# Kernel optimization log

Measured on AMD Instinct MI355X. Metric: run time of the kernel, lower is better.

Reference implementation:

```python
import jax, jax.numpy as jnp
import numpy as np

C = 3.0e8
WAVE_LAMBDA = 0.0038
PI = float(np.pi)


def _grid(size, resolution, x_val):
    edge_left = [-i for i in range(1, size, 2)][::-1]
    edge_right = [i for i in range(1, size, 2)]
    edge = edge_left + edge_right
    if size % 2 == 1:
        edge = [i for i in range(-(size - 1), size, 2)]
    edge = np.array(edge, dtype=np.float32) * resolution / 2.0
    wx, wy = np.meshgrid(edge, edge)
    wz = np.zeros((size, size), dtype=np.float32)
    pos = np.stack((wz, wx, wy), 2).reshape(size * size, 3).astype(np.float32)
    pos[:, 0] = x_val
    return pos


def setup_inputs() -> dict:
    key = jax.random.key(0)
    k1, k2, k3 = jax.random.split(key, 3)
    lam = WAVE_LAMBDA
    f = np.arange(77e9, 81e9 + 1e9, 1e9, dtype=np.float32)  # [5]
    tx = np.array([[0, -8 * lam, 0], [0, -6 * lam, 0], [0, -4 * lam, 0], [0, -2 * lam, 0],
                   [0, 0, 0], [0, 2 * lam, 0], [0, 4 * lam, 0], [0, 6 * lam, 0], [0, 8 * lam, 0],
                   [0, -2.5 * lam, -3 * lam], [0, -3.0 * lam, -2 * lam], [0, -3.5 * lam, -0.5 * lam]],
                  dtype=np.float32)  # [12,3]
    rx = np.array([[0, -16 * lam, -0.066], [0, -15.5 * lam, -0.066], [0, -15 * lam, -0.066],
                   [0, -14.5 * lam, -0.066], [0, -10.5 * lam, -0.066], [0, -10 * lam, -0.066],
                   [0, -9.5 * lam, -0.066], [0, -9 * lam, -0.066], [0, 7 * lam, -0.066],
                   [0, 7.5 * lam, -0.066], [0, 8 * lam, -0.066], [0, 8.5 * lam, -0.066],
                   [0, 9 * lam, -0.066], [0, 9.5 * lam, -0.066], [0, 10 * lam, -0.066],
                   [0, 10.5 * lam, -0.066]], dtype=np.float32)  # [16,3]
    meta = _grid(60, 0.0015, 0.1)     # [3600,3]
    scene = _grid(20, 0.0015, 0.3)    # [400,3] (resolution reassigned to 0.0015 in torch init)
    # trainable params
    meta_theta = jax.random.uniform(k1, (3600, 1), jnp.float32,
                                    minval=-PI, maxval=20 * PI / 180.0)
    w = jax.random.normal(k2, (5, 6, 12), jnp.float32)
    T = jax.random.normal(k3, (400, 128), jnp.float32)
    return {"T": T, "w": w, "meta_theta": meta_theta, "f": jnp.asarray(f),
            "tx_positions": jnp.asarray(tx), "rx_positions": jnp.asarray(rx),
            "meta_positions": jnp.asarray(meta), "scene_positions": jnp.asarray(scene)}


def _channel(locs_start, locs_end, f):
    # pairwise distance [Ns,Ne], then complex channel [F,Ns,Ne]
    d = jnp.linalg.norm(locs_start[:, None, :] - locs_end[None, :, :], axis=2)
    return (0.001 / d ** 2) * jnp.exp(-1j * 2 * PI * f[:, None, None] * d / C)


def reference(T, w, meta_theta, f, tx_positions, rx_positions, meta_positions, scene_positions):
    theta = jnp.clip(meta_theta, -PI, 20 * PI / 180.0)[:, 0]   # [M]
    phase = jnp.exp(1j * theta)                                # [M]
    pri = jnp.exp(1j * w)                                      # [F,6,Tx]
    H1 = _channel(tx_positions, meta_positions, f)             # [F,Tx,M]
    H2 = _channel(meta_positions, scene_positions, f)          # [F,M,S]
    H3 = _channel(scene_positions, meta_positions, f)          # [F,S,M]
    H4 = _channel(meta_positions, rx_positions, f)             # [F,M,Rx]
    A = jnp.einsum('fkt,ftm->fkm', pri, H1)                    # [F,6,M]
    A = A * phase[None, None, :]
    A = jnp.einsum('fkm,fms->fks', A, H2)                      # [F,6,S]
    # diag_embed(A) @ H3  ==  per-row scaling of H3 (no dense SxS diag needed)
    A = A[..., None] * H3[:, None, :, :]                       # [F,6,S,M]
    A = A * phase[None, None, None, :]
    A = jnp.einsum('fksm,fmr->fksr', A, H4)                    # [F,6,S,Rx]
    A = jnp.transpose(A, (3, 0, 1, 2))                         # [Rx,F,6,S]
    A = jnp.tile(A, (1, 1, 12, 1))                             # [Rx,F,72,S]
    A = A.reshape(-1, A.shape[3])                              # [Rx*F*72, S]
    T_complex = T.astype(jnp.complex64)
    mic_data = A @ T_complex                                   # [Rx*F*72, B]
    s_A = jnp.concatenate([A.real, A.imag], axis=0)            # [2*Rx*F*72, S]
    s_mic = jnp.concatenate([mic_data.real, mic_data.imag], axis=0)[..., None]
    return (s_A, s_mic)
```

## Files before the change

kernel.cpp:

```cpp
#include <hip/hip_runtime.h>
#include <hip/hip_bf16.h>
#include <math.h>

#define F_N 5
#define K_N 6
#define T_N 12
#define M_N 3600
#define S_N 400
#define R_N 16
#define B_N 128

#define PI_F 3.14159265358979f
#define CLIP_HI 0.3490658503988659f
#define NEG_TWO_PI_OVER_C (-6.283185307179586f / 3.0e8f)
#define INV_TWO_PI 0.15915494309189535f

#define SA_BASE   0
#define MIC_BASE  4608000

#define NK 113
#define KP (NK * 32)
#define SPK 8
#define W_ELEMS  (5 * 48 * KP)
#define C_ELEMS  (SPK * 5 * 48 * 800)
#define WS_NEED  ((size_t)W_ELEMS * 2 + (size_t)C_ELEMS * 4)

typedef __attribute__((ext_vector_type(8))) short bf16x8;
typedef __attribute__((ext_vector_type(4))) short s16x4;
typedef __attribute__((ext_vector_type(4))) float f32x4;

__device__ __forceinline__ void fast_sincos(float x, float* s, float* c) {
    float r = x * INV_TWO_PI;
    r -= floorf(r);
    *s = __builtin_amdgcn_sinf(r);
    *c = __builtin_amdgcn_cosf(r);
}

__device__ __forceinline__ ushort f2bf(float x) {
    unsigned u = __float_as_uint(x);
    unsigned r = u + 0x7fffu + ((u >> 16) & 1u);
    return (ushort)(r >> 16);
}


__global__ __launch_bounds__(256) void stage_kernel(
    const float* __restrict__ w, const float* __restrict__ meta_theta,
    const float* __restrict__ fin, const float* __restrict__ txp,
    const float* __restrict__ rxp, const float* __restrict__ metap,
    __hip_bfloat16* __restrict__ Wbf)
{
    const int tid = threadIdx.x;
    const int blk = blockIdx.x;

    __shared__ float pri[K_N * T_N * 2];
    __shared__ float txs[T_N * 3];
    __shared__ float rxs[R_N * 3];
    const int f = blk / 15;
    const int mblk = blk % 15;

    if (tid < K_N * T_N) {
        float sv, cv; fast_sincos(w[f * (K_N * T_N) + tid], &sv, &cv);
        pri[tid * 2] = cv; pri[tid * 2 + 1] = sv;
    }
    if (tid >= 64 && tid < 64 + T_N * 3) txs[tid - 64] = txp[tid - 64];
    if (tid >= 128 && tid < 128 + R_N * 3) rxs[tid - 128] = rxp[tid - 128];
    __syncthreads();

    const int m = mblk * 256 + tid;
    if (m >= KP) return;
    __hip_bfloat16* wb = Wbf + ((size_t)(f * NK + (m >> 5)) * 48) * 32 + (m & 31);

    if (m >= M_N) {
        for (int row = 0; row < 48; ++row) wb[row * 32] = __float2bfloat16(0.f);
        return;
    }

    const float px = metap[m * 3 + 0];
    const float py = metap[m * 3 + 1];
    const float pz = metap[m * 3 + 2];
    const float coef = NEG_TWO_PI_OVER_C * fin[f];

    float th = meta_theta[m];
    th = fminf(fmaxf(th, -PI_F), CLIP_HI);
    float phs, phc; fast_sincos(th, &phs, &phc);

    float hre[T_N], him[T_N];
#pragma unroll
    for (int t = 0; t < T_N; ++t) {
        float dx = txs[t * 3 + 0] - px, dy = txs[t * 3 + 1] - py, dz = txs[t * 3 + 2] - pz;
        float d = sqrtf(dx * dx + dy * dy + dz * dz);
        float amp = 1e-3f / (d * d);
        float sv, cv; fast_sincos(coef * d, &sv, &cv);
        hre[t] = amp * cv; him[t] = amp * sv;
    }
#pragma unroll
    for (int k = 0; k < K_N; ++k) {
        float ar = 0.f, ai = 0.f;
#pragma unroll
        for (int t = 0; t < T_N; ++t) {
            float pr = pri[(k * T_N + t) * 2], pim = pri[(k * T_N + t) * 2 + 1];
            ar += pr * hre[t] - pim * him[t];
            ai += pr * him[t] + pim * hre[t];
        }
        wb[k * 32]        = __float2bfloat16(ar * phc - ai * phs);
        wb[(22 + k) * 32] = __float2bfloat16(ar * phs + ai * phc);
    }
#pragma unroll
    for (int r = 0; r < R_N; ++r) {
        float dx = rxs[r * 3 + 0] - px, dy = rxs[r * 3 + 1] - py, dz = rxs[r * 3 + 2] - pz;
        float d = sqrtf(dx * dx + dy * dy + dz * dz);
        float amp = 1e-3f / (d * d);
        float sv, cv; fast_sincos(coef * d, &sv, &cv);
        float cr = amp * cv, ci = amp * sv;
        wb[(6 + r) * 32]  = __float2bfloat16(cr * phc - ci * phs);
        wb[(28 + r) * 32] = __float2bfloat16(cr * phs + ci * phc);
    }
#pragma unroll
    for (int row = 44; row < 48; ++row) wb[row * 32] = __float2bfloat16(0.f);
}

__global__ __launch_bounds__(128) void gemm_fused_kernel(
    const ushort* __restrict__ Wbf, const float* __restrict__ fin,
    const float* __restrict__ metap, const float* __restrict__ scenep,
    float* __restrict__ Cp)
{
    const int blk = blockIdx.x;
    const int f = blk / (25 * SPK);
    const int rem = blk % (25 * SPK);
    const int nblk = rem / SPK;
    const int ksp = rem % SPK;
    const int tid = threadIdx.x;
    const int wave = tid >> 6;
    const int lane = tid & 63;
    const int quad = lane >> 4;
    const int l16 = lane & 15;

    const int kbeg = (ksp == 0) ? 0 : (15 + 14 * (ksp - 1));
    const int kcnt = (ksp == 0) ? 15 : 14;

    const int p  = tid & 15;
    const int kq = tid >> 4;
    const int s  = nblk * 16 + p;
    const float coef = NEG_TWO_PI_OVER_C * fin[f];
    const float sx = scenep[s * 3 + 0];
    const float sy = scenep[s * 3 + 1];
    const float sz = scenep[s * 3 + 2];

    __shared__ ushort tile[2][32][40];

    const int n = nblk * 32 + wave * 16 + l16;

    f32x4 acc0 = {0.f, 0.f, 0.f, 0.f};
    f32x4 acc1 = {0.f, 0.f, 0.f, 0.f};
    f32x4 acc2 = {0.f, 0.f, 0.f, 0.f};

    auto produce = [&](int buf, int kb) {
        const int k0 = kq * 4;
        const int mb = kb * 32 + k0;
        s16x4 r4, i4;
#pragma unroll
        for (int j = 0; j < 4; ++j) {
            const int m = mb + j;
            float re = 0.f, im = 0.f;
            if (m < M_N) {
                float px = metap[m * 3 + 0], py = metap[m * 3 + 1], pz = metap[m * 3 + 2];
                float dx = px - sx, dy = py - sy, dz = pz - sz;
                float d = sqrtf(dx * dx + dy * dy + dz * dz);
                float amp = 1e-3f / (d * d);
                float sv, cv; fast_sincos(coef * d, &sv, &cv);
                re = amp * cv; im = amp * sv;
            }
            r4[j] = (short)f2bf(re);
            i4[j] = (short)f2bf(im);
        }
        *(s16x4*)&tile[buf][2 * p][k0]     = r4;
        *(s16x4*)&tile[buf][2 * p + 1][k0] = i4;
    };

    produce(0, kbeg);
    __syncthreads();

    for (int kk = 0; kk < kcnt; ++kk) {
        const int kb = kbeg + kk;
        const int cur = kk & 1;
        if (kk + 1 < kcnt) produce(cur ^ 1, kb + 1);

        bf16x8 b = *(const bf16x8*)&tile[cur][wave * 16 + l16][quad * 8];
        const ushort* wbase = Wbf + ((size_t)(f * NK + kb) * 48) * 32 + quad * 8;
        bf16x8 a0 = *(const bf16x8*)(wbase + (size_t)l16 * 32);
        bf16x8 a1 = *(const bf16x8*)(wbase + (size_t)(16 + l16) * 32);
        bf16x8 a2 = *(const bf16x8*)(wbase + (size_t)(32 + l16) * 32);
        acc0 = __builtin_amdgcn_mfma_f32_16x16x32_bf16(a0, b, acc0, 0, 0, 0);
        acc1 = __builtin_amdgcn_mfma_f32_16x16x32_bf16(a1, b, acc1, 0, 0, 0);
        acc2 = __builtin_amdgcn_mfma_f32_16x16x32_bf16(a2, b, acc2, 0, 0, 0);
        __syncthreads();
    }

    float* cb = Cp + ((size_t)(ksp * 5 + f) * 48) * 800;
#pragma unroll
    for (int i = 0; i < 4; ++i) {
        int row = quad * 4 + i;
        cb[(size_t)row * 800 + n]        = acc0[i];
        cb[(size_t)(16 + row) * 800 + n] = acc1[i];
        cb[(size_t)(32 + row) * 800 + n] = acc2[i];
    }
}

__device__ __forceinline__ void combineC(const float* __restrict__ Cp, int f, int row,
                                         int s, float* re, float* im) {
    float r = 0.f, i = 0.f;
#pragma unroll
    for (int pp = 0; pp < SPK; ++pp) {
        const float* c = Cp + ((size_t)(pp * 5 + f) * 48) * 800;
        float arr = c[(size_t)row * 800 + 2 * s];
        float ari = c[(size_t)row * 800 + 2 * s + 1];
        float air = c[(size_t)(22 + row) * 800 + 2 * s];
        float aii = c[(size_t)(22 + row) * 800 + 2 * s + 1];
        r += arr - aii;
        i += ari + air;
    }
    *re = r; *im = i;
}

#define SA_BLOCKS 750
__global__ __launch_bounds__(256) void epilogue2_kernel(
    const float* __restrict__ Cp, const float* __restrict__ T,
    float* __restrict__ out)
{
    __shared__ float cre[S_N], cim[S_N];
    __shared__ float pR[256], pI[256];
    const int tid = threadIdx.x;
    const int blk = blockIdx.x;

    if (blk < SA_BLOCKS) {
        int i = blk * 256 + tid;
        int s = i % S_N; int rest = i / S_N;
        int k = rest % K_N; rest /= K_N;
        int f = rest % F_N; int r = rest / F_N;

        float ar, ai, br, bi;
        combineC(Cp, f, k, s, &ar, &ai);
        combineC(Cp, f, 6 + r, s, &br, &bi);
        float cr = ar * br - ai * bi;
        float ci = ar * bi + ai * br;

        int base = (r * F_N + f) * 72;
#pragma unroll
        for (int j = 0; j < 12; ++j) {
            int row = base + j * K_N + k;
            out[SA_BASE + (size_t)row * S_N + s] = cr;
            out[SA_BASE + (size_t)(5760 + row) * S_N + s] = ci;
        }
    } else {
        int bk = blk - SA_BLOCKS;
        int k = bk % K_N;
        int f = (bk / K_N) % F_N;
        int r = bk / (K_N * F_N);

        for (int s = tid; s < S_N; s += 256) {
            float ar, ai, br, bi;
            combineC(Cp, f, k, s, &ar, &ai);
            combineC(Cp, f, 6 + r, s, &br, &bi);
            cre[s] = ar * br - ai * bi;
            cim[s] = ar * bi + ai * br;
        }
        __syncthreads();

        const int b = tid & 127;
        const int hs = tid >> 7;
        float accR = 0.f, accI = 0.f;
        const int sBeg = hs * 200, sEnd = sBeg + 200;
#pragma unroll 4
        for (int s = sBeg; s < sEnd; ++s) {
            float tv = T[s * B_N + b];
            accR += cre[s] * tv;
            accI += cim[s] * tv;
        }
        pR[tid] = accR; pI[tid] = accI;
        __syncthreads();
        if (tid < 128) {
            accR = pR[tid] + pR[tid + 128];
            accI = pI[tid] + pI[tid + 128];
            int base = (r * F_N + f) * 72;
#pragma unroll
            for (int j = 0; j < 12; ++j) {
                int row = base + j * K_N + k;
                out[MIC_BASE + (size_t)row * B_N + b] = accR;
                out[MIC_BASE + (size_t)(5760 + row) * B_N + b] = accI;
            }
        }
    }
}

__global__ __launch_bounds__(256) void prep_kernel(
    const float* __restrict__ w, const float* __restrict__ meta_theta,
    const float* __restrict__ fin, const float* __restrict__ txp,
    const float* __restrict__ rxp, const float* __restrict__ metap,
    float* __restrict__ A1, float* __restrict__ H4p)
{
    __shared__ float pri[K_N * T_N * 2];
    __shared__ float txs[T_N * 3];
    __shared__ float rxs[R_N * 3];
    const int tid = threadIdx.x;
    const int f = blockIdx.x / 15;
    const int mblk = blockIdx.x % 15;

    if (tid < K_N * T_N) {
        float sv, cv; fast_sincos(w[f * (K_N * T_N) + tid], &sv, &cv);
        pri[tid * 2] = cv; pri[tid * 2 + 1] = sv;
    }
    if (tid >= 64 && tid < 64 + T_N * 3) txs[tid - 64] = txp[tid - 64];
    if (tid >= 128 && tid < 128 + R_N * 3) rxs[tid - 128] = rxp[tid - 128];
    __syncthreads();

    const int m = mblk * 256 + tid;
    if (m >= M_N) return;

    const float px = metap[m * 3 + 0];
    const float py = metap[m * 3 + 1];
    const float pz = metap[m * 3 + 2];
    const float coef = NEG_TWO_PI_OVER_C * fin[f];

    float th = meta_theta[m];
    th = fminf(fmaxf(th, -PI_F), CLIP_HI);
    float phs, phc; fast_sincos(th, &phs, &phc);

    float hre[T_N], him[T_N];
#pragma unroll
    for (int t = 0; t < T_N; ++t) {
        float dx = txs[t * 3 + 0] - px, dy = txs[t * 3 + 1] - py, dz = txs[t * 3 + 2] - pz;
        float d = sqrtf(dx * dx + dy * dy + dz * dz);
        float amp = 1e-3f / (d * d);
        float sv, cv; fast_sincos(coef * d, &sv, &cv);
        hre[t] = amp * cv; him[t] = amp * sv;
    }
    float* a1 = A1 + ((size_t)f * M_N + m) * (K_N * 2);
#pragma unroll
    for (int k = 0; k < K_N; ++k) {
        float ar = 0.f, ai = 0.f;
#pragma unroll
        for (int t = 0; t < T_N; ++t) {
            float pr = pri[(k * T_N + t) * 2], pim = pri[(k * T_N + t) * 2 + 1];
            ar += pr * hre[t] - pim * him[t];
            ai += pr * him[t] + pim * hre[t];
        }
        a1[k * 2]     = ar * phc - ai * phs;
        a1[k * 2 + 1] = ar * phs + ai * phc;
    }
    float* h4 = H4p + ((size_t)f * M_N + m) * (R_N * 2);
#pragma unroll
    for (int r = 0; r < R_N; ++r) {
        float dx = rxs[r * 3 + 0] - px, dy = rxs[r * 3 + 1] - py, dz = rxs[r * 3 + 2] - pz;
        float d = sqrtf(dx * dx + dy * dy + dz * dz);
        float amp = 1e-3f / (d * d);
        float sv, cv; fast_sincos(coef * d, &sv, &cv);
        float cr = amp * cv, ci = amp * sv;
        h4[r * 2]     = cr * phc - ci * phs;
        h4[r * 2 + 1] = cr * phs + ci * phc;
    }
}

__global__ __launch_bounds__(256, 2) void main_kernel(
    const float* __restrict__ fin, const float* __restrict__ metap,
    const float* __restrict__ scenep, const float* __restrict__ A1,
    const float* __restrict__ H4p, float* __restrict__ A2, float* __restrict__ Bm)
{
    const int f = blockIdx.x / 200;
    const int sq = blockIdx.x % 200;
    const int s0 = 2 * sq, s1 = s0 + 1;
    const int tid = threadIdx.x;

    const float coef = NEG_TWO_PI_OVER_C * fin[f];
    const float sx0 = scenep[s0 * 3], sy0 = scenep[s0 * 3 + 1], sz0 = scenep[s0 * 3 + 2];
    const float sx1 = scenep[s1 * 3], sy1 = scenep[s1 * 3 + 1], sz1 = scenep[s1 * 3 + 2];

    float acc[88];
#pragma unroll
    for (int i = 0; i < 88; ++i) acc[i] = 0.f;

    const float4* a1base = (const float4*)(A1 + (size_t)f * M_N * (K_N * 2));
    const float4* h4base = (const float4*)(H4p + (size_t)f * M_N * (R_N * 2));

    for (int m = tid; m < M_N; m += 256) {
        float px = metap[m * 3 + 0], py = metap[m * 3 + 1], pz = metap[m * 3 + 2];
        float dx0 = px - sx0, dy0 = py - sy0, dz0 = pz - sz0;
        float d0 = sqrtf(dx0 * dx0 + dy0 * dy0 + dz0 * dz0);
        float dx1 = px - sx1, dy1 = py - sy1, dz1 = pz - sz1;
        float d1 = sqrtf(dx1 * dx1 + dy1 * dy1 + dz1 * dz1);
        float sv0, cv0, sv1, cv1;
        fast_sincos(coef * d0, &sv0, &cv0);
        fast_sincos(coef * d1, &sv1, &cv1);
        float amp0 = 1e-3f / (d0 * d0), amp1 = 1e-3f / (d1 * d1);
        float h2r0 = amp0 * cv0, h2i0 = amp0 * sv0;
        float h2r1 = amp1 * cv1, h2i1 = amp1 * sv1;

        const float4* a1 = a1base + (size_t)m * 3;
#pragma unroll
        for (int q = 0; q < 3; ++q) {
            float4 v = a1[q];
            acc[4 * q + 0] += v.x * h2r0 - v.y * h2i0;
            acc[4 * q + 1] += v.x * h2i0 + v.y * h2r0;
            acc[4 * q + 2] += v.z * h2r0 - v.w * h2i0;
            acc[4 * q + 3] += v.z * h2i0 + v.w * h2r0;
            acc[44 + 4 * q + 0] += v.x * h2r1 - v.y * h2i1;
            acc[44 + 4 * q + 1] += v.x * h2i1 + v.y * h2r1;
            acc[44 + 4 * q + 2] += v.z * h2r1 - v.w * h2i1;
            acc[44 + 4 * q + 3] += v.z * h2i1 + v.w * h2r1;
        }
        const float4* h4 = h4base + (size_t)m * 8;
#pragma unroll
        for (int q = 0; q < 8; ++q) {
            float4 v = h4[q];
            acc[12 + 4 * q + 0] += v.x * h2r0 - v.y * h2i0;
            acc[12 + 4 * q + 1] += v.x * h2i0 + v.y * h2r0;
            acc[12 + 4 * q + 2] += v.z * h2r0 - v.w * h2i0;
            acc[12 + 4 * q + 3] += v.z * h2i0 + v.w * h2r0;
            acc[56 + 4 * q + 0] += v.x * h2r1 - v.y * h2i1;
            acc[56 + 4 * q + 1] += v.x * h2i1 + v.y * h2r1;
            acc[56 + 4 * q + 2] += v.z * h2r1 - v.w * h2i1;
            acc[56 + 4 * q + 3] += v.z * h2i1 + v.w * h2r1;
        }
    }

#pragma unroll
    for (int off = 32; off > 0; off >>= 1) {
#pragma unroll
        for (int i = 0; i < 88; ++i) acc[i] += __shfl_down(acc[i], off);
    }
    __shared__ float red[4][88];
    const int wave = tid >> 6, lane = tid & 63;
    if (lane == 0) {
#pragma unroll
        for (int i = 0; i < 88; ++i) red[wave][i] = acc[i];
    }
    __syncthreads();
    if (tid < 88) {
        float v = red[0][tid] + red[1][tid] + red[2][tid] + red[3][tid];
        int half = tid / 44, slot = tid - 44 * half;
        int s = half ? s1 : s0;
        if (slot < 12) {
            int k = slot >> 1, c = slot & 1;
            A2[(((size_t)f * K_N + k) * S_N + s) * 2 + c] = v;
        } else {
            int j = slot - 12; int r = j >> 1, c = j & 1;
            Bm[(((size_t)f * S_N + s) * R_N + r) * 2 + c] = v;
        }
    }
}

__global__ __launch_bounds__(256) void epilogue_kernel(
    const float* __restrict__ A2, const float* __restrict__ Bm,
    const float* __restrict__ T, float* __restrict__ out)
{
    __shared__ float cre[S_N], cim[S_N];
    __shared__ float pR[256], pI[256];
    const int tid = threadIdx.x;
    const int blk = blockIdx.x;

    if (blk < SA_BLOCKS) {
        int i = blk * 256 + tid;
        int s = i % S_N; int rest = i / S_N;
        int k = rest % K_N; rest /= K_N;
        int f = rest % F_N; int r = rest / F_N;

        float ar = A2[((f * K_N + k) * S_N + s) * 2];
        float ai = A2[((f * K_N + k) * S_N + s) * 2 + 1];
        float br = Bm[((f * S_N + s) * R_N + r) * 2];
        float bi = Bm[((f * S_N + s) * R_N + r) * 2 + 1];
        float cr = ar * br - ai * bi;
        float ci = ar * bi + ai * br;

        int base = (r * F_N + f) * 72;
#pragma unroll
        for (int j = 0; j < 12; ++j) {
            int row = base + j * K_N + k;
            out[SA_BASE + (size_t)row * S_N + s] = cr;
            out[SA_BASE + (size_t)(5760 + row) * S_N + s] = ci;
        }
    } else {
        int bk = blk - SA_BLOCKS;
        int k = bk % K_N;
        int f = (bk / K_N) % F_N;
        int r = bk / (K_N * F_N);

        for (int s = tid; s < S_N; s += 256) {
            float ar = A2[((f * K_N + k) * S_N + s) * 2];
            float ai = A2[((f * K_N + k) * S_N + s) * 2 + 1];
            float br = Bm[((f * S_N + s) * R_N + r) * 2];
            float bi = Bm[((f * S_N + s) * R_N + r) * 2 + 1];
            cre[s] = ar * br - ai * bi;
            cim[s] = ar * bi + ai * br;
        }
        __syncthreads();

        const int b = tid & 127;
        const int hs = tid >> 7;
        float accR = 0.f, accI = 0.f;
        const int sBeg = hs * 200, sEnd = sBeg + 200;
#pragma unroll 4
        for (int s = sBeg; s < sEnd; ++s) {
            float tv = T[s * B_N + b];
            accR += cre[s] * tv;
            accI += cim[s] * tv;
        }
        pR[tid] = accR; pI[tid] = accI;
        __syncthreads();
        if (tid < 128) {
            accR = pR[tid] + pR[tid + 128];
            accI = pI[tid] + pI[tid + 128];
            int base = (r * F_N + f) * 72;
#pragma unroll
            for (int j = 0; j < 12; ++j) {
                int row = base + j * K_N + k;
                out[MIC_BASE + (size_t)row * B_N + b] = accR;
                out[MIC_BASE + (size_t)(5760 + row) * B_N + b] = accI;
            }
        }
    }
}

extern "C" void kernel_launch(void* const* d_in, const int* in_sizes, int n_in,
                              void* d_out, int out_size, void* d_ws, size_t ws_size,
                              hipStream_t stream) {
    const float* T  = (const float*)d_in[0];
    const float* w  = (const float*)d_in[1];
    const float* th = (const float*)d_in[2];
    const float* fr = (const float*)d_in[3];
    const float* tx = (const float*)d_in[4];
    const float* rx = (const float*)d_in[5];
    const float* mp = (const float*)d_in[6];
    const float* sp = (const float*)d_in[7];

    float* out = (float*)d_out;

    if (ws_size >= WS_NEED) {
        __hip_bfloat16* Wbf = (__hip_bfloat16*)d_ws;
        float* Cp = (float*)((char*)d_ws + (size_t)W_ELEMS * 2);

        stage_kernel<<<75, 256, 0, stream>>>(w, th, fr, tx, rx, mp, Wbf);
        gemm_fused_kernel<<<5 * 25 * SPK, 128, 0, stream>>>((const ushort*)Wbf, fr, mp, sp, Cp);
        epilogue2_kernel<<<SA_BLOCKS + 480, 256, 0, stream>>>(Cp, T, out);
    } else {
        float* ws  = (float*)d_ws;
        float* A1  = ws;
        float* H4p = ws + 216000;
        float* A2  = ws + 792000;
        float* Bm  = ws + 816000;

        prep_kernel<<<75, 256, 0, stream>>>(w, th, fr, tx, rx, mp, A1, H4p);
        main_kernel<<<F_N * 200, 256, 0, stream>>>(fr, mp, sp, A1, H4p, A2, Bm);
        epilogue_kernel<<<SA_BLOCKS + 480, 256, 0, stream>>>(A2, Bm, T, out);
    }
}
```

Before: 128.0 us.

## Fuse stage, GEMM and epilogue into one cooperative persistent kernel

Merges the weight-packing, split-K GEMM and epilogue kernels into a single cooperative launch with grid-wide barriers between phases, running two GEMM work items per 256-thread block and looping the epilogue over a 500-block grid. Pads the K dimension so each split-K slice gets an equal tile count. This removes inter-kernel launch gaps and tail effects at the cost of grid sync overhead, extra padded GEMM work, and reduced occupancy constraints from the cooperative grid size; falls back to the three-kernel path if the cooperative launch fails.

```diff
diff --git a/kernel.cpp b/kernel.cpp
--- a/kernel.cpp
+++ b/kernel.cpp
@@ -1,5 +1,6 @@
 #include <hip/hip_runtime.h>
 #include <hip/hip_bf16.h>
+#include <hip/hip_cooperative_groups.h>
 #include <math.h>
 
 #define F_N 5
@@ -18,12 +19,17 @@
 #define SA_BASE   0
 #define MIC_BASE  4608000
 
-#define NK 113
+#define NK 120
 #define KP (NK * 32)
 #define SPK 8
+#define KCNT (NK / SPK)
 #define W_ELEMS  (5 * 48 * KP)
 #define C_ELEMS  (SPK * 5 * 48 * 800)
 #define WS_NEED  ((size_t)W_ELEMS * 2 + (size_t)C_ELEMS * 4)
+
+#define GRID_BLOCKS 500
+#define SA_WORKS 750
+#define EPI_WORKS 1230
 
 typedef __attribute__((ext_vector_type(8))) short bf16x8;
 typedef __attribute__((ext_vector_type(4))) short s16x4;
@@ -43,18 +49,15 @@
 }
 
 
-__global__ __launch_bounds__(256) void stage_kernel(
+__device__ __forceinline__ void do_wpack(int blk, int tid,
     const float* __restrict__ w, const float* __restrict__ meta_theta,
     const float* __restrict__ fin, const float* __restrict__ txp,
     const float* __restrict__ rxp, const float* __restrict__ metap,
-    __hip_bfloat16* __restrict__ Wbf)
-{
-    const int tid = threadIdx.x;
-    const int blk = blockIdx.x;
-
-    __shared__ float pri[K_N * T_N * 2];
-    __shared__ float txs[T_N * 3];
-    __shared__ float rxs[R_N * 3];
+    ushort* __restrict__ Wbf, char* smem)
+{
+    float* pri = (float*)smem;
+    float* txs = pri + 2 * K_N * T_N;
+    float* rxs = txs + T_N * 3;
     const int f = blk / 15;
     const int mblk = blk % 15;
 
@@ -67,11 +70,10 @@
     __syncthreads();
 
     const int m = mblk * 256 + tid;
-    if (m >= KP) return;
-    __hip_bfloat16* wb = Wbf + ((size_t)(f * NK + (m >> 5)) * 48) * 32 + (m & 31);
+    ushort* wb = Wbf + ((size_t)(f * NK + (m >> 5)) * 48) * 32 + (m & 31);
 
     if (m >= M_N) {
-        for (int row = 0; row < 48; ++row) wb[row * 32] = __float2bfloat16(0.f);
+        for (int row = 0; row < 48; ++row) wb[row * 32] = 0;
         return;
     }
 
@@ -102,8 +104,8 @@
             ar += pr * hre[t] - pim * him[t];
             ai += pr * him[t] + pim * hre[t];
         }
-        wb[k * 32]        = __float2bfloat16(ar * phc - ai * phs);
-        wb[(22 + k) * 32] = __float2bfloat16(ar * phs + ai * phc);
+        wb[k * 32]        = f2bf(ar * phc - ai * phs);
+        wb[(22 + k) * 32] = f2bf(ar * phs + ai * phc);
     }
 #pragma unroll
     for (int r = 0; r < R_N; ++r) {
@@ -112,41 +114,37 @@
         float amp = 1e-3f / (d * d);
         float sv, cv; fast_sincos(coef * d, &sv, &cv);
         float cr = amp * cv, ci = amp * sv;
-        wb[(6 + r) * 32]  = __float2bfloat16(cr * phc - ci * phs);
-        wb[(28 + r) * 32] = __float2bfloat16(cr * phs + ci * phc);
-    }
-#pragma unroll
-    for (int row = 44; row < 48; ++row) wb[row * 32] = __float2bfloat16(0.f);
-}
-
-__global__ __launch_bounds__(128) void gemm_fused_kernel(
-    const ushort* __restrict__ Wbf, const float* __restrict__ fin,
-    const float* __restrict__ metap, const float* __restrict__ scenep,
-    float* __restrict__ Cp)
-{
-    const int blk = blockIdx.x;
-    const int f = blk / (25 * SPK);
-    const int rem = blk % (25 * SPK);
+        wb[(6 + r) * 32]  = f2bf(cr * phc - ci * phs);
+        wb[(28 + r) * 32] = f2bf(cr * phs + ci * phc);
+    }
+#pragma unroll
+    for (int row = 44; row < 48; ++row) wb[row * 32] = 0;
+}
+
+__device__ __forceinline__ void do_gemm_half(int wk, int t128,
+    const float* __restrict__ fin, const float* __restrict__ metap,
+    const float* __restrict__ scenep, const ushort* __restrict__ Wbf,
+    float* __restrict__ Cp, char* tilebase)
+{
+    const int f = wk / 200;
+    const int rem = wk % 200;
     const int nblk = rem / SPK;
     const int ksp = rem % SPK;
-    const int tid = threadIdx.x;
-    const int wave = tid >> 6;
-    const int lane = tid & 63;
+    const int wave = t128 >> 6;
+    const int lane = t128 & 63;
     const int quad = lane >> 4;
     const int l16 = lane & 15;
-
-    const int kbeg = (ksp == 0) ? 0 : (15 + 14 * (ksp - 1));
-    const int kcnt = (ksp == 0) ? 15 : 14;
-
-    const int p  = tid & 15;
-    const int kq = tid >> 4;
+    const int kbeg = ksp * KCNT;
+
+    ushort (*tile)[32][40] = (ushort (*)[32][40])tilebase;
+
+    const int p  = t128 & 15;
+    const int kq = t128 >> 4;
     const int s  = nblk * 16 + p;
     const float coef = NEG_TWO_PI_OVER_C * fin[f];
     const float sx = scenep[s * 3 + 0];
     const float sy = scenep[s * 3 + 1];
     const float sz = scenep[s * 3 + 2];
-
-    __shared__ ushort tile[2][32][40];
 
     const int n = nblk * 32 + wave * 16 + l16;
 
@@ -180,10 +178,10 @@
     produce(0, kbeg);
     __syncthreads();
 
-    for (int kk = 0; kk < kcnt; ++kk) {
+    for (int kk = 0; kk < KCNT; ++kk) {
         const int kb = kbeg + kk;
         const int cur = kk & 1;
-        if (kk + 1 < kcnt) produce(cur ^ 1, kb + 1);
+        if (kk + 1 < KCNT) produce(cur ^ 1, kb + 1);
 
         bf16x8 b = *(const bf16x8*)&tile[cur][wave * 16 + l16][quad * 8];
         const ushort* wbase = Wbf + ((size_t)(f * NK + kb) * 48) * 32 + quad * 8;
@@ -222,18 +220,12 @@
     *re = r; *im = i;
 }
 
-#define SA_BLOCKS 750
-__global__ __launch_bounds__(256) void epilogue2_kernel(
+__device__ __forceinline__ void do_epilogue(int w, int tid,
     const float* __restrict__ Cp, const float* __restrict__ T,
-    float* __restrict__ out)
-{
-    __shared__ float cre[S_N], cim[S_N];
-    __shared__ float pR[256], pI[256];
-    const int tid = threadIdx.x;
-    const int blk = blockIdx.x;
-
-    if (blk < SA_BLOCKS) {
-        int i = blk * 256 + tid;
+    float* __restrict__ out, char* smem)
+{
+    if (w < SA_WORKS) {
+        int i = w * 256 + tid;
         int s = i % S_N; int rest = i / S_N;
         int k = rest % K_N; rest /= K_N;
         int f = rest % F_N; int r = rest / F_N;
@@ -252,10 +244,15 @@
             out[SA_BASE + (size_t)(5760 + row) * S_N + s] = ci;
         }
     } else {
-        int bk = blk - SA_BLOCKS;
+        int bk = w - SA_WORKS;
         int k = bk % K_N;
         int f = (bk / K_N) % F_N;
         int r = bk / (K_N * F_N);
+
+        float* cre = (float*)smem;
+        float* cim = cre + S_N;
+        float* pR  = cim + S_N;
+        float* pI  = pR + 256;
 
         for (int s = tid; s < S_N; s += 256) {
             float ar, ai, br, bi;
@@ -292,6 +289,63 @@
     }
 }
 
+__global__ __launch_bounds__(256, 2) void fused_all_kernel(
+    const float* __restrict__ w, const float* __restrict__ meta_theta,
+    const float* __restrict__ fin, const float* __restrict__ txp,
+    const float* __restrict__ rxp, const float* __restrict__ metap,
+    const float* __restrict__ scenep, ushort* __restrict__ Wbf,
+    float* __restrict__ Cp, const float* __restrict__ T,
+    float* __restrict__ out)
+{
+    __shared__ __align__(16) char smem[10240];
+    const int tid = threadIdx.x;
+    const int blk = blockIdx.x;
+
+    if (blk < 75)
+        do_wpack(blk, tid, w, meta_theta, fin, txp, rxp, metap, Wbf, smem);
+    cooperative_groups::this_grid().sync();
+
+    {
+        const int half = tid >> 7;
+        do_gemm_half(blk * 2 + half, tid & 127, fin, metap, scenep, Wbf, Cp,
+                     smem + half * 5120);
+    }
+    cooperative_groups::this_grid().sync();
+
+    for (int wv = blk; wv < EPI_WORKS; wv += GRID_BLOCKS) {
+        __syncthreads();
+        do_epilogue(wv, tid, Cp, T, out, smem);
+    }
+}
+
+__global__ __launch_bounds__(256) void stage_kernel(
+    const float* __restrict__ w, const float* __restrict__ meta_theta,
+    const float* __restrict__ fin, const float* __restrict__ txp,
+    const float* __restrict__ rxp, const float* __restrict__ metap,
+    ushort* __restrict__ Wbf)
+{
+    __shared__ __align__(16) char smem[1024];
+    do_wpack(blockIdx.x, threadIdx.x, w, meta_theta, fin, txp, rxp, metap, Wbf, smem);
+}
+
+__global__ __launch_bounds__(128) void gemm_fused_kernel(
+    const ushort* __restrict__ Wbf, const float* __restrict__ fin,
+    const float* __restrict__ metap, const float* __restrict__ scenep,
+    float* __restrict__ Cp)
+{
+    __shared__ __align__(16) char tile[5120];
+    do_gemm_half(blockIdx.x, threadIdx.x, fin, metap, scenep, Wbf, Cp, tile);
+}
+
+__global__ __launch_bounds__(256) void epilogue2_kernel(
+    const float* __restrict__ Cp, const float* __restrict__ T,
+    float* __restrict__ out)
+{
+    __shared__ __align__(16) char smem[5248];
+    do_epilogue(blockIdx.x, threadIdx.x, Cp, T, out, smem);
+}
+
+#define SA_BLOCKS 750
 __global__ __launch_bounds__(256) void prep_kernel(
     const float* __restrict__ w, const float* __restrict__ meta_theta,
     const float* __restrict__ fin, const float* __restrict__ txp,
@@ -534,12 +588,20 @@
     float* out = (float*)d_out;
 
     if (ws_size >= WS_NEED) {
-        __hip_bfloat16* Wbf = (__hip_bfloat16*)d_ws;
+        ushort* Wbf = (ushort*)d_ws;
         float* Cp = (float*)((char*)d_ws + (size_t)W_ELEMS * 2);
 
-        stage_kernel<<<75, 256, 0, stream>>>(w, th, fr, tx, rx, mp, Wbf);
-        gemm_fused_kernel<<<5 * 25 * SPK, 128, 0, stream>>>((const ushort*)Wbf, fr, mp, sp, Cp);
-        epilogue2_kernel<<<SA_BLOCKS + 480, 256, 0, stream>>>(Cp, T, out);
+        void* args[] = { (void*)&w, (void*)&th, (void*)&fr, (void*)&tx, (void*)&rx,
+                         (void*)&mp, (void*)&sp, (void*)&Wbf, (void*)&Cp,
+                         (void*)&T, (void*)&out };
+        hipError_t e = hipLaunchCooperativeKernel(
+            (const void*)fused_all_kernel, dim3(GRID_BLOCKS), dim3(256),
+            args, 0u, stream);
+        if (e != hipSuccess) {
+            stage_kernel<<<75, 256, 0, stream>>>(w, th, fr, tx, rx, mp, Wbf);
+            gemm_fused_kernel<<<1000, 128, 0, stream>>>(Wbf, fr, mp, sp, Cp);
+            epilogue2_kernel<<<EPI_WORKS, 256, 0, stream>>>(Cp, T, out);
+        }
     } else {
         float* ws  = (float*)d_ws;
         float* A1  = ws;
```

Measured after the change: 253.4 us. +97.9%, slower.

## Reduce split-K partials with atomics into a single zeroed buffer

Applied to the files above, without the earlier changes.

The GEMM's split-K partial results are now accumulated with atomicAdd into one C buffer instead of SPK separate slices. Extra stage blocks zero that buffer first, so the epilogue reads a single slice instead of summing eight. NK is padded to 120 so every K split gets an equal 15 iterations. This trades workspace traffic and the epilogue reduction for atomic contention, extra zeroing work and nondeterministic summation order.

```diff
diff --git a/kernel.cpp b/kernel.cpp
--- a/kernel.cpp
+++ b/kernel.cpp
@@ -18,12 +18,17 @@
 #define SA_BASE   0
 #define MIC_BASE  4608000
 
-#define NK 113
+#define NK 120
 #define KP (NK * 32)
 #define SPK 8
+#define KCNT (NK / SPK)
 #define W_ELEMS  (5 * 48 * KP)
-#define C_ELEMS  (SPK * 5 * 48 * 800)
+#define C_ELEMS  (5 * 48 * 800)
 #define WS_NEED  ((size_t)W_ELEMS * 2 + (size_t)C_ELEMS * 4)
+
+#define STAGE_BLOCKS 105
+#define SA_WORKS 750
+#define EPI_WORKS 1230
 
 typedef __attribute__((ext_vector_type(8))) short bf16x8;
 typedef __attribute__((ext_vector_type(4))) short s16x4;
@@ -42,15 +47,23 @@
     return (ushort)(r >> 16);
 }
 
-
 __global__ __launch_bounds__(256) void stage_kernel(
     const float* __restrict__ w, const float* __restrict__ meta_theta,
     const float* __restrict__ fin, const float* __restrict__ txp,
     const float* __restrict__ rxp, const float* __restrict__ metap,
-    __hip_bfloat16* __restrict__ Wbf)
+    ushort* __restrict__ Wbf, float* __restrict__ Cp)
 {
     const int tid = threadIdx.x;
     const int blk = blockIdx.x;
+
+    if (blk >= 75) {
+        float4* cz = (float4*)Cp;
+        const int t = (blk - 75) * 256 + tid;
+        for (int i = t; i < C_ELEMS / 4; i += 30 * 256) {
+            cz[i] = make_float4(0.f, 0.f, 0.f, 0.f);
+        }
+        return;
+    }
 
     __shared__ float pri[K_N * T_N * 2];
     __shared__ float txs[T_N * 3];
@@ -67,11 +80,10 @@
     __syncthreads();
 
     const int m = mblk * 256 + tid;
-    if (m >= KP) return;
-    __hip_bfloat16* wb = Wbf + ((size_t)(f * NK + (m >> 5)) * 48) * 32 + (m & 31);
+    ushort* wb = Wbf + ((size_t)(f * NK + (m >> 5)) * 48) * 32 + (m & 31);
 
     if (m >= M_N) {
-        for (int row = 0; row < 48; ++row) wb[row * 32] = __float2bfloat16(0.f);
+        for (int row = 0; row < 48; ++row) wb[row * 32] = 0;
         return;
     }
 
@@ -102,8 +114,8 @@
             ar += pr * hre[t] - pim * him[t];
             ai += pr * him[t] + pim * hre[t];
         }
-        wb[k * 32]        = __float2bfloat16(ar * phc - ai * phs);
-        wb[(22 + k) * 32] = __float2bfloat16(ar * phs + ai * phc);
+        wb[k * 32]        = f2bf(ar * phc - ai * phs);
+        wb[(22 + k) * 32] = f2bf(ar * phs + ai * phc);
     }
 #pragma unroll
     for (int r = 0; r < R_N; ++r) {
@@ -112,11 +124,11 @@
         float amp = 1e-3f / (d * d);
         float sv, cv; fast_sincos(coef * d, &sv, &cv);
         float cr = amp * cv, ci = amp * sv;
-        wb[(6 + r) * 32]  = __float2bfloat16(cr * phc - ci * phs);
-        wb[(28 + r) * 32] = __float2bfloat16(cr * phs + ci * phc);
-    }
-#pragma unroll
-    for (int row = 44; row < 48; ++row) wb[row * 32] = __float2bfloat16(0.f);
+        wb[(6 + r) * 32]  = f2bf(cr * phc - ci * phs);
+        wb[(28 + r) * 32] = f2bf(cr * phs + ci * phc);
+    }
+#pragma unroll
+    for (int row = 44; row < 48; ++row) wb[row * 32] = 0;
 }
 
 __global__ __launch_bounds__(128) void gemm_fused_kernel(
@@ -124,29 +136,27 @@
     const float* __restrict__ metap, const float* __restrict__ scenep,
     float* __restrict__ Cp)
 {
-    const int blk = blockIdx.x;
-    const int f = blk / (25 * SPK);
-    const int rem = blk % (25 * SPK);
+    const int wk = blockIdx.x;
+    const int f = wk / 200;
+    const int rem = wk % 200;
     const int nblk = rem / SPK;
     const int ksp = rem % SPK;
-    const int tid = threadIdx.x;
-    const int wave = tid >> 6;
-    const int lane = tid & 63;
+    const int t128 = threadIdx.x;
+    const int wave = t128 >> 6;
+    const int lane = t128 & 63;
     const int quad = lane >> 4;
     const int l16 = lane & 15;
-
-    const int kbeg = (ksp == 0) ? 0 : (15 + 14 * (ksp - 1));
-    const int kcnt = (ksp == 0) ? 15 : 14;
-
-    const int p  = tid & 15;
-    const int kq = tid >> 4;
+    const int kbeg = ksp * KCNT;
+
+    __shared__ ushort tile[2][32][40];
+
+    const int p  = t128 & 15;
+    const int kq = t128 >> 4;
     const int s  = nblk * 16 + p;
     const float coef = NEG_TWO_PI_OVER_C * fin[f];
     const float sx = scenep[s * 3 + 0];
     const float sy = scenep[s * 3 + 1];
     const float sz = scenep[s * 3 + 2];
-
-    __shared__ ushort tile[2][32][40];
 
     const int n = nblk * 32 + wave * 16 + l16;
 
@@ -180,10 +190,10 @@
     produce(0, kbeg);
     __syncthreads();
 
-    for (int kk = 0; kk < kcnt; ++kk) {
+    for (int kk = 0; kk < KCNT; ++kk) {
         const int kb = kbeg + kk;
         const int cur = kk & 1;
-        if (kk + 1 < kcnt) produce(cur ^ 1, kb + 1);
+        if (kk + 1 < KCNT) produce(cur ^ 1, kb + 1);
 
         bf16x8 b = *(const bf16x8*)&tile[cur][wave * 16 + l16][quad * 8];
         const ushort* wbase = Wbf + ((size_t)(f * NK + kb) * 48) * 32 + quad * 8;
@@ -196,33 +206,27 @@
         __syncthreads();
     }
 
-    float* cb = Cp + ((size_t)(ksp * 5 + f) * 48) * 800;
+    float* cb = Cp + (size_t)f * 48 * 800;
 #pragma unroll
     for (int i = 0; i < 4; ++i) {
         int row = quad * 4 + i;
-        cb[(size_t)row * 800 + n]        = acc0[i];
-        cb[(size_t)(16 + row) * 800 + n] = acc1[i];
-        cb[(size_t)(32 + row) * 800 + n] = acc2[i];
+        atomicAdd(&cb[(size_t)row * 800 + n],        acc0[i]);
+        atomicAdd(&cb[(size_t)(16 + row) * 800 + n], acc1[i]);
+        atomicAdd(&cb[(size_t)(32 + row) * 800 + n], acc2[i]);
     }
 }
 
 __device__ __forceinline__ void combineC(const float* __restrict__ Cp, int f, int row,
                                          int s, float* re, float* im) {
-    float r = 0.f, i = 0.f;
-#pragma unroll
-    for (int pp = 0; pp < SPK; ++pp) {
-        const float* c = Cp + ((size_t)(pp * 5 + f) * 48) * 800;
-        float arr = c[(size_t)row * 800 + 2 * s];
-        float ari = c[(size_t)row * 800 + 2 * s + 1];
-        float air = c[(size_t)(22 + row) * 800 + 2 * s];
-        float aii = c[(size_t)(22 + row) * 800 + 2 * s + 1];
-        r += arr - aii;
-        i += ari + air;
-    }
-    *re = r; *im = i;
-}
-
-#define SA_BLOCKS 750
+    const float* c = Cp + (size_t)f * 48 * 800;
+    float arr = c[(size_t)row * 800 + 2 * s];
+    float ari = c[(size_t)row * 800 + 2 * s + 1];
+    float air = c[(size_t)(22 + row) * 800 + 2 * s];
+    float aii = c[(size_t)(22 + row) * 800 + 2 * s + 1];
+    *re = arr - aii;
+    *im = ari + air;
+}
+
 __global__ __launch_bounds__(256) void epilogue2_kernel(
     const float* __restrict__ Cp, const float* __restrict__ T,
     float* __restrict__ out)
@@ -232,7 +236,7 @@
     const int tid = threadIdx.x;
     const int blk = blockIdx.x;
 
-    if (blk < SA_BLOCKS) {
+    if (blk < SA_WORKS) {
         int i = blk * 256 + tid;
         int s = i % S_N; int rest = i / S_N;
         int k = rest % K_N; rest /= K_N;
@@ -252,7 +256,7 @@
             out[SA_BASE + (size_t)(5760 + row) * S_N + s] = ci;
         }
     } else {
-        int bk = blk - SA_BLOCKS;
+        int bk = blk - SA_WORKS;
         int k = bk % K_N;
         int f = (bk / K_N) % F_N;
         int r = bk / (K_N * F_N);
@@ -292,6 +296,7 @@
     }
 }
 
+#define SA_BLOCKS 750
 __global__ __launch_bounds__(256) void prep_kernel(
     const float* __restrict__ w, const float* __restrict__ meta_theta,
     const float* __restrict__ fin, const float* __restrict__ txp,
@@ -534,12 +539,12 @@
     float* out = (float*)d_out;
 
     if (ws_size >= WS_NEED) {
-        __hip_bfloat16* Wbf = (__hip_bfloat16*)d_ws;
+        ushort* Wbf = (ushort*)d_ws;
         float* Cp = (float*)((char*)d_ws + (size_t)W_ELEMS * 2);
 
-        stage_kernel<<<75, 256, 0, stream>>>(w, th, fr, tx, rx, mp, Wbf);
-        gemm_fused_kernel<<<5 * 25 * SPK, 128, 0, stream>>>((const ushort*)Wbf, fr, mp, sp, Cp);
-        epilogue2_kernel<<<SA_BLOCKS + 480, 256, 0, stream>>>(Cp, T, out);
+        stage_kernel<<<STAGE_BLOCKS, 256, 0, stream>>>(w, th, fr, tx, rx, mp, Wbf, Cp);
+        gemm_fused_kernel<<<1000, 128, 0, stream>>>(Wbf, fr, mp, sp, Cp);
+        epilogue2_kernel<<<EPI_WORKS, 256, 0, stream>>>(Cp, T, out);
     } else {
         float* ws  = (float*)d_ws;
         float* A1  = ws;
```

Result: faster. 121.3 us (-5.2%).
